# Optimization experiments

Measured on AMD Instinct MI355X. Metric: run time of the kernel, lower is better.

## Reference

```python
import jax, jax.numpy as jnp
import numpy as np

B, N, C, H, K = 4, 16384, 256, 8, 64
D = C // H
EPS = 1e-8

def setup_inputs() -> dict:
    key = jax.random.key(0)
    ks = jax.random.split(key, 6)
    scale = 0.02
    return {
        "voxel_features": jax.random.normal(ks[0], (B, N, C), dtype=jnp.float32),
        "cluster_assignments": jax.random.uniform(ks[1], (B, N, K), dtype=jnp.float32),
        "w_qkv": jax.random.normal(ks[2], (C, 3 * C), dtype=jnp.float32) * scale,
        "w_proj": jax.random.normal(ks[3], (C, C), dtype=jnp.float32) * scale,
        "b_proj": jnp.zeros((C,), dtype=jnp.float32),
        "cluster_bias": jax.random.normal(ks[4], (K, K), dtype=jnp.float32) * scale,
    }

def reference(voxel_features, cluster_assignments, w_qkv, w_proj, b_proj, cluster_bias):
    b, n, c = voxel_features.shape
    h, d = H, c // H
    A = cluster_assignments                                  # (B,N,K)
    qkv = (voxel_features @ w_qkv).reshape(b, n, 3, h, d)    # (B,N,3,H,D)
    q = jnp.moveaxis(qkv[:, :, 0], 1, 2)                     # (B,H,N,D)
    k = jnp.moveaxis(qkv[:, :, 1], 1, 2)
    v = jnp.moveaxis(qkv[:, :, 2], 1, 2)
    # cluster mass per (batch, cluster)
    denom = A.sum(axis=1) + EPS                              # (B,K)
    # cluster-pooled K/V: contraction over N (the huge broadcast-sum in torch)
    k_cluster = jnp.einsum('bnk,bhnd->bhkd', A, k) / denom[:, None, :, None]
    v_cluster = jnp.einsum('bnk,bhnd->bhkd', A, v) / denom[:, None, :, None]
    attn = jnp.einsum('bhnd,bhkd->bhnk', q, k_cluster) * (d ** -0.5)
    bias = jnp.einsum('bnk,kl->bnl', A, cluster_bias)        # (B,N,K)
    attn = jax.nn.softmax(attn + bias[:, None, :, :], axis=-1)
    x = jnp.einsum('bhnk,bhkd->bhnd', attn, v_cluster)       # (B,H,N,D)
    x = jnp.moveaxis(x, 1, 2).reshape(b, n, c)               # (B,N,C)
    return x @ w_proj + b_proj
```

## Files before the change

kernel.cpp:

```cpp
#include <hip/hip_runtime.h>

#define NTOK 16384
#define BATCH 4

typedef __attribute__((ext_vector_type(8))) short bf16x8;
typedef __attribute__((ext_vector_type(8))) unsigned short ushort8;
typedef __attribute__((ext_vector_type(4))) float f32x4;

__device__ __forceinline__ unsigned short f2bf(float f) {
  union { float f; unsigned int u; } c; c.f = f;
  unsigned int r = c.u + 0x7fff + ((c.u >> 16) & 1);
  return (unsigned short)(r >> 16);
}

__global__ __launch_bounds__(256) void zero_f(float* __restrict__ p, int n) {
  int i = blockIdx.x * 256 + threadIdx.x;
  if (i < n) p[i] = 0.f;
}

__global__ __launch_bounds__(256) void convx2(const float* __restrict__ voxel,
                                              const float* __restrict__ A,
                                              unsigned short* __restrict__ xb,
                                              unsigned short* __restrict__ Ab) {
  for (int i = blockIdx.x * 256 + threadIdx.x; i < 2621440; i += gridDim.x * 256) {
    const float* src; unsigned short* dst; int j;
    if (i < 2097152) { j = i; src = voxel; dst = xb; }
    else { j = i - 2097152; src = A; dst = Ab; }
    float4 a = *(const float4*)(src + 8 * (size_t)j);
    float4 b = *(const float4*)(src + 8 * (size_t)j + 4);
    ushort8 o;
    o[0] = f2bf(a.x); o[1] = f2bf(a.y); o[2] = f2bf(a.z); o[3] = f2bf(a.w);
    o[4] = f2bf(b.x); o[5] = f2bf(b.y); o[6] = f2bf(b.z); o[7] = f2bf(b.w);
    *(ushort8*)(dst + 8 * (size_t)j) = o;
  }
}

__global__ __launch_bounds__(256) void convw(const float* __restrict__ w_qkv,
                                             const float* __restrict__ w_proj,
                                             const float* __restrict__ cb,
                                             unsigned short* __restrict__ wqT,
                                             unsigned short* __restrict__ wpT,
                                             unsigned short* __restrict__ cbbT) {
  int n = blockIdx.x, k = threadIdx.x;
  if (n < 768) wqT[n * 256 + k] = f2bf(w_qkv[(size_t)k * 768 + n]);
  else if (n < 1024) wpT[(n - 768) * 256 + k] = f2bf(w_proj[(size_t)k * 256 + (n - 768)]);
  else if (k < 64) {
    for (int j = 0; j < 64; ++j) cbbT[k * 64 + j] = f2bf(cb[j * 64 + k]);
  }
}

template <int ADD_BIAS, int C_BF16>
__global__ __launch_bounds__(256, 2) void gemm_mfma(const unsigned short* __restrict__ Ab,
                                                    const unsigned short* __restrict__ BT,
                                                    const float* __restrict__ bias,
                                                    void* __restrict__ Cv,
                                                    int N, int K, int lda) {
  __shared__ unsigned short As[2][128][72];
  __shared__ unsigned short Bs[2][128][72];
  const int tid = threadIdx.x;
  int flat = blockIdx.y * gridDim.x + blockIdx.x;
  int xc = flat & 7, t = flat >> 3;
  int gx = gridDim.x, ypx = gridDim.y >> 3;
  int bx = t % gx, by = xc * ypx + t / gx;
  const int bn = bx * 128, bm = by * 128;
  const int lane = tid & 63;
  const int wv = tid >> 6;
  const int wm = wv & 1, wn = wv >> 1;
  const int m16 = lane & 15, quad = lane >> 4;

  const int srow = tid >> 1;
  const int scol = (tid & 1) * 32;

  ushort8 ra[4][4], rb[4][4];
  {
    const unsigned short* ga = Ab + (size_t)(bm + srow) * lda + scol;
    const unsigned short* gb = BT + (size_t)(bn + srow) * K + scol;
#pragma unroll
    for (int kt = 0; kt < 4; ++kt)
#pragma unroll
      for (int i = 0; i < 4; ++i) {
        ra[kt][i] = *(const ushort8*)(ga + kt * 64 + 8 * i);
        rb[kt][i] = *(const ushort8*)(gb + kt * 64 + 8 * i);
      }
  }

  f32x4 acc[4][4];
#pragma unroll
  for (int r = 0; r < 4; ++r)
#pragma unroll
    for (int c = 0; c < 4; ++c) acc[r][c] = (f32x4){0.f, 0.f, 0.f, 0.f};

#pragma unroll
  for (int kt = 0; kt < 4; ++kt) {
    const int bufi = kt & 1;
#pragma unroll
    for (int i = 0; i < 4; ++i) {
      *(ushort8*)&As[bufi][srow][scol + 8 * i] = ra[kt][i];
      *(ushort8*)&Bs[bufi][srow][scol + 8 * i] = rb[kt][i];
    }
    __syncthreads();
#pragma unroll
    for (int ks = 0; ks < 64; ks += 32) {
      bf16x8 af[4], bf[4];
#pragma unroll
      for (int r = 0; r < 4; ++r)
        af[r] = *(const bf16x8*)&As[bufi][wm * 64 + r * 16 + m16][ks + quad * 8];
#pragma unroll
      for (int c = 0; c < 4; ++c)
        bf[c] = *(const bf16x8*)&Bs[bufi][wn * 64 + c * 16 + m16][ks + quad * 8];
#pragma unroll
      for (int r = 0; r < 4; ++r)
#pragma unroll
        for (int c = 0; c < 4; ++c)
          acc[r][c] = __builtin_amdgcn_mfma_f32_16x16x32_bf16(af[r], bf[c], acc[r][c], 0, 0, 0);
    }
  }

#pragma unroll
  for (int c = 0; c < 4; ++c) {
    int col = bn + wn * 64 + c * 16 + m16;
    float bv = ADD_BIAS ? bias[col] : 0.f;
#pragma unroll
    for (int r = 0; r < 4; ++r) {
      int row0 = bm + wm * 64 + r * 16 + quad * 4;
#pragma unroll
      for (int i = 0; i < 4; ++i) {
        if (C_BF16)
          ((unsigned short*)Cv)[(size_t)(row0 + i) * N + col] = f2bf(acc[r][c][i] + bv);
        else
          ((float*)Cv)[(size_t)(row0 + i) * N + col] = acc[r][c][i] + bv;
      }
    }
  }
}

__global__ __launch_bounds__(256) void pool_mfma(const float* __restrict__ A,
                                                 const unsigned short* __restrict__ qkv,
                                                 float* __restrict__ part) {
  __shared__ unsigned short At[64][40];
  __shared__ unsigned short KVt[128][40];
  const int tid = threadIdx.x;
  const int tch = blockIdx.x, cblk = blockIdx.y, b = blockIdx.z;
  const int w = tid >> 6, lane = tid & 63;
  const int m16 = lane & 15, quad = lane >> 4;
  const size_t row0 = (size_t)b * NTOK + (size_t)tch * 256;
  const int cb0 = cblk * 128;

  f32x4 acc[4][2];
#pragma unroll
  for (int r = 0; r < 4; ++r)
#pragma unroll
    for (int c = 0; c < 2; ++c) acc[r][c] = (f32x4){0.f, 0.f, 0.f, 0.f};

  ushort8 pkv[2];
  float4 pav[2];
  auto loadG = [&](int t0) {
#pragma unroll
    for (int u = 0; u < 2; ++u) {
      int idx = tid + u * 256;
      int tok = idx & 31, g = idx >> 5;
      pkv[u] = *(const ushort8*)(qkv + (row0 + t0 + tok) * 768 + 256 + cb0 + g * 8);
      pav[u] = *(const float4*)(A + (row0 + t0 + tok) * 64 + g * 4);
    }
  };
  loadG(0);

  for (int ks = 0; ks < 8; ++ks) {
    __syncthreads();
#pragma unroll
    for (int u = 0; u < 2; ++u) {
      int idx = tid + u * 256;
      int tok = idx & 31, g = idx >> 5;
#pragma unroll
      for (int i = 0; i < 8; ++i) KVt[g * 8 + i][tok] = (unsigned short)pkv[u][i];
      At[g * 4 + 0][tok] = f2bf(pav[u].x);
      At[g * 4 + 1][tok] = f2bf(pav[u].y);
      At[g * 4 + 2][tok] = f2bf(pav[u].z);
      At[g * 4 + 3][tok] = f2bf(pav[u].w);
    }
    __syncthreads();
    if (ks + 1 < 8) loadG((ks + 1) * 32);
    bf16x8 af[4], bfr[2];
#pragma unroll
    for (int r = 0; r < 4; ++r) af[r] = *(const bf16x8*)&At[r * 16 + m16][quad * 8];
#pragma unroll
    for (int c = 0; c < 2; ++c) bfr[c] = *(const bf16x8*)&KVt[w * 32 + c * 16 + m16][quad * 8];
#pragma unroll
    for (int r = 0; r < 4; ++r)
#pragma unroll
      for (int c = 0; c < 2; ++c)
        acc[r][c] = __builtin_amdgcn_mfma_f32_16x16x32_bf16(af[r], bfr[c], acc[r][c], 0, 0, 0);
  }

  float* pp = part + (((size_t)b * 64 + tch) * 64) * 512 + cb0;
#pragma unroll
  for (int r = 0; r < 4; ++r)
#pragma unroll
    for (int c = 0; c < 2; ++c)
#pragma unroll
      for (int i = 0; i < 4; ++i) {
        int cl = r * 16 + quad * 4 + i;
        int ch = w * 32 + c * 16 + m16;
        pp[(size_t)cl * 512 + ch] = acc[r][c][i];
      }
}

__global__ __launch_bounds__(256) void pool2(const float* __restrict__ part,
                                             const float* __restrict__ asum,
                                             unsigned short* __restrict__ kcb,
                                             unsigned short* __restrict__ vcbT) {
  int id = blockIdx.x * 256 + threadIdx.x;
  int c = id & 511;
  int cl = (id >> 9) & 63;
  int b = id >> 15;
  const float* pp = part + ((size_t)b * 64 * 64 + cl) * 512 + c;
  float s = 0.f;
#pragma unroll 4
  for (int t = 0; t < 64; ++t) s += pp[(size_t)t * 32768];
  float denom = asum[b * 64 + cl] + 1e-8f;
  int p = c >> 8, h = (c >> 5) & 7, d = c & 31;
  if (p == 0)
    kcb[(((size_t)b * 8 + h) * 64 + cl) * 32 + d] = f2bf(s * 0.17677669529663687f / denom);
  else
    vcbT[(((size_t)b * 8 + h) * 32 + d) * 64 + cl] = f2bf(s / denom);
}

__global__ __launch_bounds__(256) void asum_kernel(const float* __restrict__ A,
                                                   float* __restrict__ asum) {
  __shared__ float red[4][64];
  const int ch = blockIdx.x, b = blockIdx.y;
  const int jq = threadIdx.x >> 6, k = threadIdx.x & 63;
  const size_t row0 = (size_t)b * NTOK + (size_t)ch * 256;
  const float* ap = A + (row0 + jq) * 64 + k;
  float s = 0.f;
#pragma unroll 4
  for (int j = 0; j < 64; ++j) s += ap[(size_t)j * 256];
  red[jq][k] = s;
  __syncthreads();
  if (threadIdx.x < 64) {
    float v = red[0][k] + red[1][k] + red[2][k] + red[3][k];
    atomicAdd(&asum[b * 64 + k], v);
  }
}

__global__ __launch_bounds__(256) void attn_mfma(const unsigned short* __restrict__ Ab,
                                                 unsigned short* __restrict__ qkv,
                                                 const unsigned short* __restrict__ kcb,
                                                 const unsigned short* __restrict__ vcbT,
                                                 const unsigned short* __restrict__ cbbT) {
  __shared__ __align__(16) char lds[38400];
  unsigned short* PA  = (unsigned short*)lds;
  unsigned short* Qs  = (unsigned short*)(lds + 18432);
  unsigned short* KCs = (unsigned short*)(lds + 28672);
  unsigned short* VTs = (unsigned short*)(lds + 33792);
  unsigned short* CBs = (unsigned short*)(lds + 28672);

  const int tid = threadIdx.x;
  const int nb = blockIdx.x, hq = blockIdx.y, b = blockIdx.z;
  const int h0 = hq * 4;
  const int w = tid >> 6, lane = tid & 63;
  const int m16 = lane & 15, quad = lane >> 4;
  const size_t row0 = (size_t)b * NTOK + (size_t)nb * 128;

  const int r2 = tid >> 1, half = tid & 1;
  const int l4 = tid >> 2, s3 = tid & 3;
  const int d8 = tid >> 3, s7 = tid & 7;

  ushort8 rA[4], rcb[2];
  {
    const unsigned short* ap = Ab + (row0 + r2) * 64 + half * 32;
#pragma unroll
    for (int u = 0; u < 4; ++u) rA[u] = *(const ushort8*)(ap + 8 * u);
    const unsigned short* cp = cbbT + l4 * 64 + s3 * 16;
    rcb[0] = *(const ushort8*)cp;
    rcb[1] = *(const ushort8*)(cp + 8);
  }
  ushort8 rq[2][2], rkc[2], rvt[2];
  {
    const unsigned short* qp = qkv + (row0 + r2) * 768 + h0 * 32 + half * 16;
    rq[0][0] = *(const ushort8*)qp;
    rq[0][1] = *(const ushort8*)(qp + 8);
    rkc[0] = *(const ushort8*)(kcb + (((size_t)b * 8 + h0) * 64 + l4) * 32 + s3 * 8);
    rvt[0] = *(const ushort8*)(vcbT + (((size_t)b * 8 + h0) * 32 + d8) * 64 + s7 * 8);
  }
#pragma unroll
  for (int u = 0; u < 4; ++u) *(ushort8*)&PA[r2 * 72 + half * 32 + 8 * u] = rA[u];
  *(ushort8*)&CBs[l4 * 72 + s3 * 16] = rcb[0];
  *(ushort8*)&CBs[l4 * 72 + s3 * 16 + 8] = rcb[1];
  __syncthreads();

  f32x4 bacc[2][4];
#pragma unroll
  for (int rt = 0; rt < 2; ++rt)
#pragma unroll
    for (int nt = 0; nt < 4; ++nt) bacc[rt][nt] = (f32x4){0.f, 0.f, 0.f, 0.f};
#pragma unroll
  for (int ks = 0; ks < 64; ks += 32) {
    bf16x8 af[2], bf[4];
#pragma unroll
    for (int rt = 0; rt < 2; ++rt)
      af[rt] = *(const bf16x8*)&PA[(w * 32 + rt * 16 + m16) * 72 + ks + quad * 8];
#pragma unroll
    for (int nt = 0; nt < 4; ++nt)
      bf[nt] = *(const bf16x8*)&CBs[(nt * 16 + m16) * 72 + ks + quad * 8];
#pragma unroll
    for (int rt = 0; rt < 2; ++rt)
#pragma unroll
      for (int nt = 0; nt < 4; ++nt)
        bacc[rt][nt] = __builtin_amdgcn_mfma_f32_16x16x32_bf16(af[rt], bf[nt], bacc[rt][nt], 0, 0, 0);
  }
  __syncthreads();

#pragma unroll
  for (int hh = 0; hh < 4; ++hh) {
    const int h = h0 + hh;
    const int cur = hh & 1;
    *(ushort8*)&Qs[r2 * 40 + half * 16] = rq[cur][0];
    *(ushort8*)&Qs[r2 * 40 + half * 16 + 8] = rq[cur][1];
    *(ushort8*)&KCs[l4 * 40 + s3 * 8] = rkc[cur];
    *(ushort8*)&VTs[d8 * 72 + s7 * 8] = rvt[cur];
    if (hh < 3) {
      const int h1 = h + 1;
      const unsigned short* qp = qkv + (row0 + r2) * 768 + h1 * 32 + half * 16;
      rq[cur ^ 1][0] = *(const ushort8*)qp;
      rq[cur ^ 1][1] = *(const ushort8*)(qp + 8);
      rkc[cur ^ 1] = *(const ushort8*)(kcb + (((size_t)b * 8 + h1) * 64 + l4) * 32 + s3 * 8);
      rvt[cur ^ 1] = *(const ushort8*)(vcbT + (((size_t)b * 8 + h1) * 32 + d8) * 64 + s7 * 8);
    }
    __syncthreads();

    f32x4 acc[2][4];
#pragma unroll
    for (int rt = 0; rt < 2; ++rt)
#pragma unroll
      for (int nt = 0; nt < 4; ++nt) acc[rt][nt] = bacc[rt][nt];
    {
      bf16x8 af[2], bf[4];
#pragma unroll
      for (int rt = 0; rt < 2; ++rt)
        af[rt] = *(const bf16x8*)&Qs[(w * 32 + rt * 16 + m16) * 40 + quad * 8];
#pragma unroll
      for (int nt = 0; nt < 4; ++nt)
        bf[nt] = *(const bf16x8*)&KCs[(nt * 16 + m16) * 40 + quad * 8];
#pragma unroll
      for (int rt = 0; rt < 2; ++rt)
#pragma unroll
        for (int nt = 0; nt < 4; ++nt)
          acc[rt][nt] = __builtin_amdgcn_mfma_f32_16x16x32_bf16(af[rt], bf[nt], acc[rt][nt], 0, 0, 0);
    }

#pragma unroll
    for (int rt = 0; rt < 2; ++rt) {
      f32x4 mxv, sv;
#pragma unroll
      for (int i = 0; i < 4; ++i)
        mxv[i] = fmaxf(fmaxf(acc[rt][0][i], acc[rt][1][i]),
                       fmaxf(acc[rt][2][i], acc[rt][3][i]));
#pragma unroll
      for (int msk = 1; msk < 16; msk <<= 1)
#pragma unroll
        for (int i = 0; i < 4; ++i) mxv[i] = fmaxf(mxv[i], __shfl_xor(mxv[i], msk));
#pragma unroll
      for (int i = 0; i < 4; ++i) sv[i] = 0.f;
#pragma unroll
      for (int nt = 0; nt < 4; ++nt)
#pragma unroll
        for (int i = 0; i < 4; ++i) {
          float e = __expf(acc[rt][nt][i] - mxv[i]);
          acc[rt][nt][i] = e;
          sv[i] += e;
        }
#pragma unroll
      for (int msk = 1; msk < 16; msk <<= 1)
#pragma unroll
        for (int i = 0; i < 4; ++i) sv[i] += __shfl_xor(sv[i], msk);
#pragma unroll
      for (int i = 0; i < 4; ++i) sv[i] = 1.f / sv[i];
#pragma unroll
      for (int nt = 0; nt < 4; ++nt)
#pragma unroll
        for (int i = 0; i < 4; ++i)
          PA[(w * 32 + rt * 16 + quad * 4 + i) * 72 + nt * 16 + m16] =
              f2bf(acc[rt][nt][i] * sv[i]);
    }

    f32x4 acc2[2][2];
#pragma unroll
    for (int rt = 0; rt < 2; ++rt)
#pragma unroll
      for (int nt = 0; nt < 2; ++nt) acc2[rt][nt] = (f32x4){0.f, 0.f, 0.f, 0.f};
#pragma unroll
    for (int kch = 0; kch < 64; kch += 32) {
      bf16x8 af2[2], bf2[2];
#pragma unroll
      for (int rt = 0; rt < 2; ++rt)
        af2[rt] = *(const bf16x8*)&PA[(w * 32 + rt * 16 + m16) * 72 + kch + quad * 8];
#pragma unroll
      for (int nt = 0; nt < 2; ++nt)
        bf2[nt] = *(const bf16x8*)&VTs[(nt * 16 + m16) * 72 + kch + quad * 8];
#pragma unroll
      for (int rt = 0; rt < 2; ++rt)
#pragma unroll
        for (int nt = 0; nt < 2; ++nt)
          acc2[rt][nt] = __builtin_amdgcn_mfma_f32_16x16x32_bf16(af2[rt], bf2[nt], acc2[rt][nt], 0, 0, 0);
    }

#pragma unroll
    for (int rt = 0; rt < 2; ++rt)
#pragma unroll
      for (int nt = 0; nt < 2; ++nt)
#pragma unroll
        for (int i = 0; i < 4; ++i) {
          int tr = w * 32 + rt * 16 + quad * 4 + i;
          int d = nt * 16 + m16;
          qkv[(row0 + tr) * 768 + h * 32 + d] = f2bf(acc2[rt][nt][i]);
        }
    __syncthreads();
  }
}

extern "C" void kernel_launch(void* const* d_in, const int* in_sizes, int n_in,
                              void* d_out, int out_size, void* d_ws, size_t ws_size,
                              hipStream_t stream) {
  const float* voxel  = (const float*)d_in[0];
  const float* A      = (const float*)d_in[1];
  const float* w_qkv  = (const float*)d_in[2];
  const float* w_proj = (const float*)d_in[3];
  const float* b_proj = (const float*)d_in[4];
  const float* cb     = (const float*)d_in[5];
  float* out = (float*)d_out;
  (void)in_sizes; (void)n_in; (void)out_size; (void)ws_size;

  char* wsb = (char*)d_ws;
  unsigned short* qkv = (unsigned short*)wsb;
  float* part = (float*)(wsb + 100663296);
  float* asum = (float*)(wsb + 100663296 + 33554432);
  unsigned short* wqT  = (unsigned short*)(wsb + 134218752);
  unsigned short* wpT  = wqT + 196608;
  unsigned short* kcb  = wpT + 65536;
  unsigned short* vcbT = kcb + 65536;
  unsigned short* cbbT = vcbT + 65536;
  unsigned short* xb = (unsigned short*)part;
  unsigned short* Ab = (unsigned short*)d_out;

  zero_f<<<1, 256, 0, stream>>>(asum, 256);
  convw<<<1025, 256, 0, stream>>>(w_qkv, w_proj, cb, wqT, wpT, cbbT);
  convx2<<<2048, 256, 0, stream>>>(voxel, A, xb, Ab);

  gemm_mfma<0, 1><<<dim3(6, 512), 256, 0, stream>>>(xb, wqT, nullptr, qkv,
                                                    768, 256, 256);

  asum_kernel<<<dim3(64, BATCH), 256, 0, stream>>>(A, asum);
  pool_mfma<<<dim3(64, 4, BATCH), 256, 0, stream>>>(A, qkv, part);
  pool2<<<512, 256, 0, stream>>>(part, asum, kcb, vcbT);

  attn_mfma<<<dim3(NTOK / 128, 2, BATCH), 256, 0, stream>>>(Ab, qkv, kcb, vcbT, cbbT);

  gemm_mfma<1, 0><<<dim3(2, 512), 256, 0, stream>>>(qkv, wpT, b_proj, out,
                                                    256, 256, 768);
}
```

Measured before the change: 270.1 us.

## Pool raw features before K/V projection and shrink QKV GEMM to Q only

Uses linearity to pool the bf16 input features by cluster assignment first (A^T X), then projects the 64 pooled rows per batch through the K/V weights in a small fp32 kernel. The large token GEMM now produces only Q, which removes two thirds of its FLOPs and its output writes. The pooling step reads bf16 A instead of fp32 A. The GEMM also gets a single shared LDS buffer, a higher occupancy bound and a coalesced epilogue staged through shared memory. The trade-off is a different rounding path, since pooling is done on bf16 inputs, plus one extra small kernel launch.

```diff
diff --git a/kernel.cpp b/kernel.cpp
--- a/kernel.cpp
+++ b/kernel.cpp
@@ -42,26 +42,28 @@
                                              unsigned short* __restrict__ wpT,
                                              unsigned short* __restrict__ cbbT) {
   int n = blockIdx.x, k = threadIdx.x;
-  if (n < 768) wqT[n * 256 + k] = f2bf(w_qkv[(size_t)k * 768 + n]);
-  else if (n < 1024) wpT[(n - 768) * 256 + k] = f2bf(w_proj[(size_t)k * 256 + (n - 768)]);
-  else if (k < 64) {
+  if (n < 256) wqT[n * 256 + k] = f2bf(w_qkv[(size_t)k * 768 + n]);
+  else if (n < 512) wpT[(n - 256) * 256 + k] = f2bf(w_proj[(size_t)k * 256 + (n - 256)]);
+  else if (n == 512 && k < 64) {
     for (int j = 0; j < 64; ++j) cbbT[k * 64 + j] = f2bf(cb[j * 64 + k]);
   }
 }
 
 template <int ADD_BIAS, int C_BF16>
-__global__ __launch_bounds__(256, 2) void gemm_mfma(const unsigned short* __restrict__ Ab,
+__global__ __launch_bounds__(256, 3) void gemm_mfma(const unsigned short* __restrict__ Ab,
                                                     const unsigned short* __restrict__ BT,
                                                     const float* __restrict__ bias,
                                                     void* __restrict__ Cv,
                                                     int N, int K, int lda) {
-  __shared__ unsigned short As[2][128][72];
-  __shared__ unsigned short Bs[2][128][72];
+  __shared__ __align__(16) unsigned short smem[2][128][72];
   const int tid = threadIdx.x;
-  int flat = blockIdx.y * gridDim.x + blockIdx.x;
-  int xc = flat & 7, t = flat >> 3;
-  int gx = gridDim.x, ypx = gridDim.y >> 3;
-  int bx = t % gx, by = xc * ypx + t / gx;
+  int bx, by;
+  if ((gridDim.y & 7) == 0) {
+    int flat = blockIdx.y * gridDim.x + blockIdx.x;
+    int xc = flat & 7, t = flat >> 3;
+    int gx = gridDim.x, ypx = gridDim.y >> 3;
+    bx = t % gx; by = xc * ypx + t / gx;
+  } else { bx = blockIdx.x; by = blockIdx.y; }
   const int bn = bx * 128, bm = by * 128;
   const int lane = tid & 63;
   const int wv = tid >> 6;
@@ -71,43 +73,50 @@
   const int srow = tid >> 1;
   const int scol = (tid & 1) * 32;
 
-  ushort8 ra[4][4], rb[4][4];
-  {
-    const unsigned short* ga = Ab + (size_t)(bm + srow) * lda + scol;
-    const unsigned short* gb = BT + (size_t)(bn + srow) * K + scol;
-#pragma unroll
-    for (int kt = 0; kt < 4; ++kt)
+  const unsigned short* ga = Ab + (size_t)(bm + srow) * lda + scol;
+  const unsigned short* gb = BT + (size_t)(bn + srow) * K + scol;
+
+  ushort8 ra[2][4], rb[2][4];
+#pragma unroll
+  for (int kt = 0; kt < 2; ++kt)
+#pragma unroll
+    for (int i = 0; i < 4; ++i) {
+      ra[kt][i] = *(const ushort8*)(ga + kt * 64 + 8 * i);
+      rb[kt][i] = *(const ushort8*)(gb + kt * 64 + 8 * i);
+    }
+
+  f32x4 acc[4][4];
+#pragma unroll
+  for (int r = 0; r < 4; ++r)
+#pragma unroll
+    for (int c = 0; c < 4; ++c) acc[r][c] = (f32x4){0.f, 0.f, 0.f, 0.f};
+
+#pragma unroll
+  for (int kt = 0; kt < 4; ++kt) {
+    const int sb = kt & 1;
+    if (kt > 0) __syncthreads();
+#pragma unroll
+    for (int i = 0; i < 4; ++i) {
+      *(ushort8*)&smem[0][srow][scol + 8 * i] = ra[sb][i];
+      *(ushort8*)&smem[1][srow][scol + 8 * i] = rb[sb][i];
+    }
+    __syncthreads();
+    if (kt < 2) {
 #pragma unroll
       for (int i = 0; i < 4; ++i) {
-        ra[kt][i] = *(const ushort8*)(ga + kt * 64 + 8 * i);
-        rb[kt][i] = *(const ushort8*)(gb + kt * 64 + 8 * i);
+        ra[sb][i] = *(const ushort8*)(ga + (kt + 2) * 64 + 8 * i);
+        rb[sb][i] = *(const ushort8*)(gb + (kt + 2) * 64 + 8 * i);
       }
-  }
-
-  f32x4 acc[4][4];
-#pragma unroll
-  for (int r = 0; r < 4; ++r)
-#pragma unroll
-    for (int c = 0; c < 4; ++c) acc[r][c] = (f32x4){0.f, 0.f, 0.f, 0.f};
-
-#pragma unroll
-  for (int kt = 0; kt < 4; ++kt) {
-    const int bufi = kt & 1;
-#pragma unroll
-    for (int i = 0; i < 4; ++i) {
-      *(ushort8*)&As[bufi][srow][scol + 8 * i] = ra[kt][i];
-      *(ushort8*)&Bs[bufi][srow][scol + 8 * i] = rb[kt][i];
-    }
-    __syncthreads();
+    }
 #pragma unroll
     for (int ks = 0; ks < 64; ks += 32) {
       bf16x8 af[4], bf[4];
 #pragma unroll
       for (int r = 0; r < 4; ++r)
-        af[r] = *(const bf16x8*)&As[bufi][wm * 64 + r * 16 + m16][ks + quad * 8];
+        af[r] = *(const bf16x8*)&smem[0][wm * 64 + r * 16 + m16][ks + quad * 8];
 #pragma unroll
       for (int c = 0; c < 4; ++c)
-        bf[c] = *(const bf16x8*)&Bs[bufi][wn * 64 + c * 16 + m16][ks + quad * 8];
+        bf[c] = *(const bf16x8*)&smem[1][wn * 64 + c * 16 + m16][ks + quad * 8];
 #pragma unroll
       for (int r = 0; r < 4; ++r)
 #pragma unroll
@@ -116,35 +125,69 @@
     }
   }
 
-#pragma unroll
-  for (int c = 0; c < 4; ++c) {
-    int col = bn + wn * 64 + c * 16 + m16;
-    float bv = ADD_BIAS ? bias[col] : 0.f;
-#pragma unroll
-    for (int r = 0; r < 4; ++r) {
-      int row0 = bm + wm * 64 + r * 16 + quad * 4;
-#pragma unroll
-      for (int i = 0; i < 4; ++i) {
-        if (C_BF16)
-          ((unsigned short*)Cv)[(size_t)(row0 + i) * N + col] = f2bf(acc[r][c][i] + bv);
-        else
-          ((float*)Cv)[(size_t)(row0 + i) * N + col] = acc[r][c][i] + bv;
+  float bv[4];
+  if (ADD_BIAS) {
+#pragma unroll
+    for (int c = 0; c < 4; ++c) bv[c] = bias[bn + wn * 64 + c * 16 + m16];
+  }
+  const int lrD = tid >> 2, cch = (tid & 3) * 32;
+  unsigned short* Csh = (unsigned short*)smem;
+  float* Csf = (float*)smem;
+#pragma unroll
+  for (int p = 0; p < 2; ++p) {
+    __syncthreads();
+    if (wm == p) {
+#pragma unroll
+      for (int r = 0; r < 4; ++r) {
+        int lr0 = r * 16 + quad * 4;
+#pragma unroll
+        for (int c = 0; c < 4; ++c) {
+          int col = wn * 64 + c * 16 + m16;
+#pragma unroll
+          for (int i = 0; i < 4; ++i) {
+            float v = acc[r][c][i] + (ADD_BIAS ? bv[c] : 0.f);
+            if (C_BF16) Csh[(lr0 + i) * 136 + col] = f2bf(v);
+            else Csf[(lr0 + i) * 132 + col] = v;
+          }
+        }
       }
     }
-  }
-}
-
-__global__ __launch_bounds__(256) void pool_mfma(const float* __restrict__ A,
-                                                 const unsigned short* __restrict__ qkv,
+    __syncthreads();
+    if (C_BF16) {
+      unsigned short* gp = (unsigned short*)Cv + (size_t)(bm + p * 64 + lrD) * N + bn + cch;
+      const unsigned short* sp = Csh + lrD * 136 + cch;
+      ushort8 t0 = *(const ushort8*)(sp + 0);
+      ushort8 t1 = *(const ushort8*)(sp + 8);
+      ushort8 t2 = *(const ushort8*)(sp + 16);
+      ushort8 t3 = *(const ushort8*)(sp + 24);
+      *(ushort8*)(gp + 0) = t0;
+      *(ushort8*)(gp + 8) = t1;
+      *(ushort8*)(gp + 16) = t2;
+      *(ushort8*)(gp + 24) = t3;
+    } else {
+      float* gp = (float*)Cv + (size_t)(bm + p * 64 + lrD) * N + bn + cch;
+      const float* sp = Csf + lrD * 132 + cch;
+      float4 t[8];
+#pragma unroll
+      for (int u = 0; u < 8; ++u) t[u] = *(const float4*)(sp + 4 * u);
+#pragma unroll
+      for (int u = 0; u < 8; ++u) *(float4*)(gp + 4 * u) = t[u];
+    }
+  }
+}
+
+__global__ __launch_bounds__(256) void pool_mfma(const unsigned short* __restrict__ Ab,
+                                                 const unsigned short* __restrict__ xb,
                                                  float* __restrict__ part) {
   __shared__ unsigned short At[64][40];
-  __shared__ unsigned short KVt[128][40];
+  __shared__ unsigned short Xt[128][40];
   const int tid = threadIdx.x;
   const int tch = blockIdx.x, cblk = blockIdx.y, b = blockIdx.z;
   const int w = tid >> 6, lane = tid & 63;
   const int m16 = lane & 15, quad = lane >> 4;
   const size_t row0 = (size_t)b * NTOK + (size_t)tch * 256;
   const int cb0 = cblk * 128;
+  const int tokL = tid & 31, gA = tid >> 5;
 
   f32x4 acc[4][2];
 #pragma unroll
@@ -152,16 +195,15 @@
 #pragma unroll
     for (int c = 0; c < 2; ++c) acc[r][c] = (f32x4){0.f, 0.f, 0.f, 0.f};
 
-  ushort8 pkv[2];
-  float4 pav[2];
+  ushort8 px[2], pa;
   auto loadG = [&](int t0) {
 #pragma unroll
     for (int u = 0; u < 2; ++u) {
       int idx = tid + u * 256;
       int tok = idx & 31, g = idx >> 5;
-      pkv[u] = *(const ushort8*)(qkv + (row0 + t0 + tok) * 768 + 256 + cb0 + g * 8);
-      pav[u] = *(const float4*)(A + (row0 + t0 + tok) * 64 + g * 4);
-    }
+      px[u] = *(const ushort8*)(xb + (row0 + t0 + tok) * 256 + cb0 + g * 8);
+    }
+    pa = *(const ushort8*)(Ab + (row0 + t0 + tokL) * 64 + gA * 8);
   };
   loadG(0);
 
@@ -172,19 +214,17 @@
       int idx = tid + u * 256;
       int tok = idx & 31, g = idx >> 5;
 #pragma unroll
-      for (int i = 0; i < 8; ++i) KVt[g * 8 + i][tok] = (unsigned short)pkv[u][i];
-      At[g * 4 + 0][tok] = f2bf(pav[u].x);
-      At[g * 4 + 1][tok] = f2bf(pav[u].y);
-      At[g * 4 + 2][tok] = f2bf(pav[u].z);
-      At[g * 4 + 3][tok] = f2bf(pav[u].w);
-    }
+      for (int i = 0; i < 8; ++i) Xt[g * 8 + i][tok] = (unsigned short)px[u][i];
+    }
+#pragma unroll
+    for (int i = 0; i < 8; ++i) At[gA * 8 + i][tokL] = (unsigned short)pa[i];
     __syncthreads();
     if (ks + 1 < 8) loadG((ks + 1) * 32);
     bf16x8 af[4], bfr[2];
 #pragma unroll
     for (int r = 0; r < 4; ++r) af[r] = *(const bf16x8*)&At[r * 16 + m16][quad * 8];
 #pragma unroll
-    for (int c = 0; c < 2; ++c) bfr[c] = *(const bf16x8*)&KVt[w * 32 + c * 16 + m16][quad * 8];
+    for (int c = 0; c < 2; ++c) bfr[c] = *(const bf16x8*)&Xt[w * 32 + c * 16 + m16][quad * 8];
 #pragma unroll
     for (int r = 0; r < 4; ++r)
 #pragma unroll
@@ -192,7 +232,7 @@
         acc[r][c] = __builtin_amdgcn_mfma_f32_16x16x32_bf16(af[r], bfr[c], acc[r][c], 0, 0, 0);
   }
 
-  float* pp = part + (((size_t)b * 64 + tch) * 64) * 512 + cb0;
+  float* pp = part + ((size_t)(b * 64 + tch) * 64) * 256 + cb0;
 #pragma unroll
   for (int r = 0; r < 4; ++r)
 #pragma unroll
@@ -201,28 +241,43 @@
       for (int i = 0; i < 4; ++i) {
         int cl = r * 16 + quad * 4 + i;
         int ch = w * 32 + c * 16 + m16;
-        pp[(size_t)cl * 512 + ch] = acc[r][c][i];
+        pp[(size_t)cl * 256 + ch] = acc[r][c][i];
       }
 }
 
 __global__ __launch_bounds__(256) void pool2(const float* __restrict__ part,
                                              const float* __restrict__ asum,
-                                             unsigned short* __restrict__ kcb,
-                                             unsigned short* __restrict__ vcbT) {
+                                             float* __restrict__ pooledX) {
   int id = blockIdx.x * 256 + threadIdx.x;
-  int c = id & 511;
-  int cl = (id >> 9) & 63;
-  int b = id >> 15;
-  const float* pp = part + ((size_t)b * 64 * 64 + cl) * 512 + c;
+  int c = id & 255, cl = (id >> 8) & 63, b = id >> 14;
+  const float* pp = part + ((size_t)(b * 64) * 64 + cl) * 256 + c;
   float s = 0.f;
 #pragma unroll 4
-  for (int t = 0; t < 64; ++t) s += pp[(size_t)t * 32768];
+  for (int t = 0; t < 64; ++t) s += pp[(size_t)t * 16384];
   float denom = asum[b * 64 + cl] + 1e-8f;
-  int p = c >> 8, h = (c >> 5) & 7, d = c & 31;
-  if (p == 0)
-    kcb[(((size_t)b * 8 + h) * 64 + cl) * 32 + d] = f2bf(s * 0.17677669529663687f / denom);
-  else
-    vcbT[(((size_t)b * 8 + h) * 32 + d) * 64 + cl] = f2bf(s / denom);
+  pooledX[(size_t)(b * 64 + cl) * 256 + c] = s / denom;
+}
+
+__global__ __launch_bounds__(256) void kvgemm(const float* __restrict__ pooledX,
+                                              const float* __restrict__ w_qkv,
+                                              unsigned short* __restrict__ kcb,
+                                              unsigned short* __restrict__ vcbT) {
+  __shared__ float px[256];
+  const int bc = blockIdx.x;
+  const int b = bc >> 6, cl = bc & 63;
+  const int tid = threadIdx.x;
+  px[tid] = pooledX[(size_t)bc * 256 + tid];
+  __syncthreads();
+  float accK = 0.f, accV = 0.f;
+#pragma unroll 8
+  for (int k = 0; k < 256; ++k) {
+    float x = px[k];
+    accK = fmaf(x, w_qkv[(size_t)k * 768 + 256 + tid], accK);
+    accV = fmaf(x, w_qkv[(size_t)k * 768 + 512 + tid], accV);
+  }
+  int h = tid >> 5, d = tid & 31;
+  kcb[(((size_t)b * 8 + h) * 64 + cl) * 32 + d] = f2bf(accK * 0.17677669529663687f);
+  vcbT[(((size_t)b * 8 + h) * 32 + d) * 64 + cl] = f2bf(accV);
 }
 
 __global__ __launch_bounds__(256) void asum_kernel(const float* __restrict__ A,
@@ -244,7 +299,7 @@
 }
 
 __global__ __launch_bounds__(256) void attn_mfma(const unsigned short* __restrict__ Ab,
-                                                 unsigned short* __restrict__ qkv,
+                                                 unsigned short* __restrict__ qb,
                                                  const unsigned short* __restrict__ kcb,
                                                  const unsigned short* __restrict__ vcbT,
                                                  const unsigned short* __restrict__ cbbT) {
@@ -277,7 +332,7 @@
   }
   ushort8 rq[2][2], rkc[2], rvt[2];
   {
-    const unsigned short* qp = qkv + (row0 + r2) * 768 + h0 * 32 + half * 16;
+    const unsigned short* qp = qb + (row0 + r2) * 256 + h0 * 32 + half * 16;
     rq[0][0] = *(const ushort8*)qp;
     rq[0][1] = *(const ushort8*)(qp + 8);
     rkc[0] = *(const ushort8*)(kcb + (((size_t)b * 8 + h0) * 64 + l4) * 32 + s3 * 8);
@@ -321,7 +376,7 @@
     *(ushort8*)&VTs[d8 * 72 + s7 * 8] = rvt[cur];
     if (hh < 3) {
       const int h1 = h + 1;
-      const unsigned short* qp = qkv + (row0 + r2) * 768 + h1 * 32 + half * 16;
+      const unsigned short* qp = qb + (row0 + r2) * 256 + h1 * 32 + half * 16;
       rq[cur ^ 1][0] = *(const ushort8*)qp;
       rq[cur ^ 1][1] = *(const ushort8*)(qp + 8);
       rkc[cur ^ 1] = *(const ushort8*)(kcb + (((size_t)b * 8 + h1) * 64 + l4) * 32 + s3 * 8);
@@ -413,7 +468,7 @@
         for (int i = 0; i < 4; ++i) {
           int tr = w * 32 + rt * 16 + quad * 4 + i;
           int d = nt * 16 + m16;
-          qkv[(row0 + tr) * 768 + h * 32 + d] = f2bf(acc2[rt][nt][i]);
+          qb[(row0 + tr) * 256 + h * 32 + d] = f2bf(acc2[rt][nt][i]);
         }
     __syncthreads();
   }
@@ -432,30 +487,32 @@
   (void)in_sizes; (void)n_in; (void)out_size; (void)ws_size;
 
   char* wsb = (char*)d_ws;
-  unsigned short* qkv = (unsigned short*)wsb;
-  float* part = (float*)(wsb + 100663296);
-  float* asum = (float*)(wsb + 100663296 + 33554432);
-  unsigned short* wqT  = (unsigned short*)(wsb + 134218752);
-  unsigned short* wpT  = wqT + 196608;
-  unsigned short* kcb  = wpT + 65536;
-  unsigned short* vcbT = kcb + 65536;
-  unsigned short* cbbT = vcbT + 65536;
-  unsigned short* xb = (unsigned short*)part;
+  unsigned short* qb       = (unsigned short*)wsb;
+  unsigned short* xb       = (unsigned short*)(wsb + 33554432);
+  float* part              = (float*)(wsb + 67108864);
+  float* asum              = (float*)(wsb + 83886080);
+  float* pooledXf          = (float*)(wsb + 83887104);
+  unsigned short* wqT      = (unsigned short*)(wsb + 84149248);
+  unsigned short* wpT      = (unsigned short*)(wsb + 84280320);
+  unsigned short* kcb      = (unsigned short*)(wsb + 84411392);
+  unsigned short* vcbT     = (unsigned short*)(wsb + 84542464);
+  unsigned short* cbbT     = (unsigned short*)(wsb + 84673536);
   unsigned short* Ab = (unsigned short*)d_out;
 
   zero_f<<<1, 256, 0, stream>>>(asum, 256);
-  convw<<<1025, 256, 0, stream>>>(w_qkv, w_proj, cb, wqT, wpT, cbbT);
+  convw<<<513, 256, 0, stream>>>(w_qkv, w_proj, cb, wqT, wpT, cbbT);
   convx2<<<2048, 256, 0, stream>>>(voxel, A, xb, Ab);
 
-  gemm_mfma<0, 1><<<dim3(6, 512), 256, 0, stream>>>(xb, wqT, nullptr, qkv,
-                                                    768, 256, 256);
+  gemm_mfma<0, 1><<<dim3(2, 512), 256, 0, stream>>>(xb, wqT, nullptr, qb,
+                                                    256, 256, 256);
 
   asum_kernel<<<dim3(64, BATCH), 256, 0, stream>>>(A, asum);
-  pool_mfma<<<dim3(64, 4, BATCH), 256, 0, stream>>>(A, qkv, part);
-  pool2<<<512, 256, 0, stream>>>(part, asum, kcb, vcbT);
-
-  attn_mfma<<<dim3(NTOK / 128, 2, BATCH), 256, 0, stream>>>(Ab, qkv, kcb, vcbT, cbbT);
-
-  gemm_mfma<1, 0><<<dim3(2, 512), 256, 0, stream>>>(qkv, wpT, b_proj, out,
-                                                    256, 256, 768);
-}
+  pool_mfma<<<dim3(64, 2, BATCH), 256, 0, stream>>>(Ab, xb, part);
+  pool2<<<256, 256, 0, stream>>>(part, asum, pooledXf);
+  kvgemm<<<256, 256, 0, stream>>>(pooledXf, w_qkv, kcb, vcbT);
+
+  attn_mfma<<<dim3(NTOK / 128, 2, BATCH), 256, 0, stream>>>(Ab, qb, kcb, vcbT, cbbT);
+
+  gemm_mfma<1, 0><<<dim3(2, 512), 256, 0, stream>>>(qb, wpT, b_proj, out,
+                                                    256, 256, 256);
+}
```

After: 274.8 us. No clear change (+1.7%).
